# Performance work log

Hardware: AMD Instinct MI355X
Metric: run time of the kernel (lower is better)

The kernel has to match this reference:

```python
import jax, jax.numpy as jnp
import numpy as np

NUM_LAYERS = 3

def setup_inputs() -> dict:
    key = jax.random.key(0)
    k1, k2, k3, k4 = jax.random.split(key, 4)
    N, D, E = 100000, 128, 3200000
    x = jax.random.normal(k1, (N, D), dtype=jnp.float32)
    edge_row = jax.random.randint(k2, (E,), 0, N, dtype=jnp.int64 if jax.config.jax_enable_x64 else jnp.int32)
    edge_col = jax.random.randint(k3, (E,), 0, N, dtype=jnp.int64 if jax.config.jax_enable_x64 else jnp.int32)
    # normalized-adjacency-like positive values
    edge_val = jax.random.uniform(k4, (E,), dtype=jnp.float32)
    return {"x": x, "edge_row": edge_row, "edge_col": edge_col, "edge_val": edge_val}

def _spmm(edge_row, edge_col, edge_val, emb, num_nodes):
    # out[r] += val * emb[c]  -- sparse adjacency @ emb
    msgs = edge_val[:, None] * emb[edge_col]          # [E, D] gather + scale
    return jax.ops.segment_sum(msgs, edge_row, num_segments=num_nodes)

def reference(x, edge_row, edge_col, edge_val):
    N = x.shape[0]
    emb = x
    acc = x  # running sum over layer embeddings (layer 0 included)
    for _ in range(NUM_LAYERS):
        emb = _spmm(edge_row, edge_col, edge_val, emb, N)
        acc = acc + emb
    # mean over (num_layers + 1) stacked embeddings, without materializing the stack
    return acc / jnp.float32(NUM_LAYERS + 1)
```

## Files before the change

kernel.cpp:

```cpp
#include <hip/hip_runtime.h>

#define DIMS 128
#define RPB 64
#define CAP 3072
#define NBK_MAX 1600
#define NBINS 1024

typedef _Float16 half_t;
typedef _Float16 half2_t __attribute__((ext_vector_type(2)));

static __device__ __forceinline__ unsigned halfbits(float v) {
    half_t h = (half_t)v;
    unsigned short us;
    __builtin_memcpy(&us, &h, 2);
    return (unsigned)us;
}

__global__ void cvt_kernel(const float* __restrict__ src, half_t* __restrict__ dst, int n2) {
    int i = blockIdx.x * blockDim.x + threadIdx.x;
    if (i >= n2) return;
    float2 v = reinterpret_cast<const float2*>(src)[i];
    half2_t h;
    h.x = (half_t)v.x;
    h.y = (half_t)v.y;
    reinterpret_cast<half2_t*>(&dst[0])[i] = h;
}

__global__ __launch_bounds__(256) void binA_kernel(
    const int* __restrict__ row, const int* __restrict__ col,
    const float* __restrict__ val, int E, int nbk,
    int* __restrict__ fill, int2* __restrict__ staged) {
    __shared__ int cnt[NBK_MAX];
    __shared__ int base[NBK_MAX];
    const int t = threadIdx.x;
    const int tile0 = blockIdx.x * 8192;
    for (int j = t; j < nbk; j += 256) cnt[j] = 0;
    __syncthreads();
    for (int k = 0; k < 8; ++k) {
        int e = tile0 + (k * 256 + t) * 4;
        if (e + 3 < E) {
            int4 r4 = *reinterpret_cast<const int4*>(&row[e]);
            atomicAdd(&cnt[r4.x >> 6], 1);
            atomicAdd(&cnt[r4.y >> 6], 1);
            atomicAdd(&cnt[r4.z >> 6], 1);
            atomicAdd(&cnt[r4.w >> 6], 1);
        } else {
            for (int j = e; j < E; ++j) atomicAdd(&cnt[row[j] >> 6], 1);
        }
    }
    __syncthreads();
    for (int j = t; j < nbk; j += 256) {
        int c = cnt[j];
        base[j] = c ? atomicAdd(&fill[j], c) : 0;
        cnt[j] = 0;
    }
    __syncthreads();
    for (int k = 0; k < 8; ++k) {
        int e = tile0 + (k * 256 + t) * 4;
        int n = (e + 3 < E) ? 4 : max(0, E - e);
        if (n == 4) {
            int4 r4 = *reinterpret_cast<const int4*>(&row[e]);
            int4 c4 = *reinterpret_cast<const int4*>(&col[e]);
            float4 v4 = *reinterpret_cast<const float4*>(&val[e]);
            int rr[4] = {r4.x, r4.y, r4.z, r4.w};
            int cc[4] = {c4.x, c4.y, c4.z, c4.w};
            float vv[4] = {v4.x, v4.y, v4.z, v4.w};
#pragma unroll
            for (int j = 0; j < 4; ++j) {
                int b = rr[j] >> 6;
                int p = base[b] + atomicAdd(&cnt[b], 1);
                if (p < CAP) {
                    unsigned hb = halfbits(vv[j]);
                    int2 pk;
                    pk.x = (int)(((unsigned)(rr[j] & 63) << 26) | ((unsigned)cc[j] << 8));
                    pk.y = (int)((hb << 16) | hb);
                    staged[(size_t)b * CAP + p] = pk;
                }
            }
        } else {
            for (int j = e; j < e + n; ++j) {
                int r = row[j];
                int b = r >> 6;
                int p = base[b] + atomicAdd(&cnt[b], 1);
                if (p < CAP) {
                    unsigned hb = halfbits(val[j]);
                    int2 pk;
                    pk.x = (int)(((unsigned)(r & 63) << 26) | ((unsigned)col[j] << 8));
                    pk.y = (int)((hb << 16) | hb);
                    staged[(size_t)b * CAP + p] = pk;
                }
            }
        }
    }
}

__global__ __launch_bounds__(512) void sort_bucket(
    const int* __restrict__ fill, int2* __restrict__ staged,
    int* __restrict__ rowinfo, int N) {
    __shared__ int2 buf[CAP];
    __shared__ int2 outb[CAP];
    __shared__ int cur[NBINS];
    __shared__ int wsum[8];
    const int b = blockIdx.x;
    const int t = threadIdx.x;
    const int w = t >> 6, lane = t & 63;
    const int cnt = min(fill[b], CAP);
    int2* gb = staged + (size_t)b * CAP;

    cur[2 * t] = 0;
    cur[2 * t + 1] = 0;
    for (int i = t; i < cnt; i += 512) buf[i] = gb[i];
    __syncthreads();
    for (int i = t; i < cnt; i += 512) {
        unsigned k = (unsigned)buf[i].x;
        int key = (int)((k >> 26) << 4) | (int)((k >> 21) & 0xF);
        atomicAdd(&cur[key], 1);
    }
    __syncthreads();
    int h0 = cur[2 * t], h1 = cur[2 * t + 1];
    int s = h0 + h1;
    int v = s;
    for (int d = 1; d < 64; d <<= 1) {
        int u = __shfl_up(v, d, 64);
        if (lane >= d) v += u;
    }
    if (lane == 63) wsum[w] = v;
    __syncthreads();
    if (t < 8) {
        int ws = wsum[t];
        int vv = ws;
        for (int d = 1; d < 8; d <<= 1) {
            int u = __shfl_up(vv, d, 64);
            if (t >= d) vv += u;
        }
        wsum[t] = vv - ws;
    }
    __syncthreads();
    int excl = wsum[w] + (v - s);
    cur[2 * t] = excl;
    cur[2 * t + 1] = excl + h0;
    __syncthreads();
    if (t < RPB) {
        int start = cur[t * 16];
        int end = (t == RPB - 1) ? cnt : cur[t * 16 + 16];
        int r = b * RPB + t;
        if (r < N) rowinfo[r] = (start << 16) | end;
    }
    __syncthreads();
    for (int i = t; i < cnt; i += 512) {
        int2 pk = buf[i];
        unsigned k = (unsigned)pk.x;
        int key = (int)((k >> 26) << 4) | (int)((k >> 21) & 0xF);
        int p = atomicAdd(&cur[key], 1);
        outb[p] = pk;
    }
    __syncthreads();
    for (int i = t; i < cnt; i += 512) gb[i] = outb[i];
}

template <int MODE>
__global__ __launch_bounds__(256) void spmm_kernel(
    const half_t* __restrict__ emb_in, const int* __restrict__ rowinfo,
    const int2* __restrict__ staged, int N,
    half_t* __restrict__ emb_out, half_t* __restrict__ acc_h,
    float* __restrict__ out) {
    int r = (blockIdx.x * blockDim.x + threadIdx.x) >> 6;
    int lane = threadIdx.x & 63;
    if (r >= N) return;
    int info = rowinfo[r];
    int start = info >> 16;
    int end = info & 0xFFFF;
    const int2* eb = staged + (size_t)(r >> 6) * CAP;
    const char* tbl = reinterpret_cast<const char*>(emb_in);
    const unsigned lane4 = (unsigned)lane << 2;

    half2_t acc[8];
#pragma unroll
    for (int k = 0; k < 8; ++k) acc[k] = (half2_t)0;

    for (int base = start; base < end; base += 64) {
        const int cnt = min(64, end - base);
        int2 myE = make_int2(0, 0);
        if (base + lane < end) myE = eb[base + lane];

        int k = 0;
        for (; k + 7 < cnt; k += 8) {
            int ex[8], ey[8];
#pragma unroll
            for (int j = 0; j < 8; ++j) {
                ex[j] = __shfl(myE.x, k + j, 64);
                ey[j] = __shfl(myE.y, k + j, 64);
            }
            half2_t tv[8];
#pragma unroll
            for (int j = 0; j < 8; ++j) {
                unsigned voff = (((unsigned)ex[j]) & 0x03FFFF00u) + lane4;
                tv[j] = *reinterpret_cast<const half2_t*>(tbl + voff);
            }
#pragma unroll
            for (int j = 0; j < 8; ++j) {
                half2_t vv = __builtin_bit_cast(half2_t, ey[j]);
                acc[j] = tv[j] * vv + acc[j];
            }
        }
        for (; k < cnt; ++k) {
            int ex = __shfl(myE.x, k, 64);
            int ey = __shfl(myE.y, k, 64);
            unsigned voff = (((unsigned)ex) & 0x03FFFF00u) + lane4;
            half2_t tvs = *reinterpret_cast<const half2_t*>(tbl + voff);
            half2_t vv = __builtin_bit_cast(half2_t, ey);
            acc[0] = tvs * vv + acc[0];
        }
    }
    half2_t a01 = acc[0] + acc[1], a23 = acc[2] + acc[3];
    half2_t a45 = acc[4] + acc[5], a67 = acc[6] + acc[7];
    half2_t a = (a01 + a23) + (a45 + a67);

    size_t o = (size_t)r * DIMS + 2 * lane;
    if (MODE == 0 || MODE == 1) {
        *reinterpret_cast<half2_t*>(&emb_out[o]) = a;
    }
    if (MODE == 0) {
        half2_t xv = *reinterpret_cast<const half2_t*>(&emb_in[o]);
        *reinterpret_cast<half2_t*>(&acc_h[o]) = xv + a;
    } else if (MODE == 1) {
        half2_t cv = *reinterpret_cast<half2_t*>(&acc_h[o]);
        *reinterpret_cast<half2_t*>(&acc_h[o]) = cv + a;
    } else {
        half2_t cv = *reinterpret_cast<half2_t*>(&acc_h[o]);
        *reinterpret_cast<float2*>(&out[o]) =
            make_float2(((float)cv.x + (float)a.x) * 0.25f,
                        ((float)cv.y + (float)a.y) * 0.25f);
    }
}


extern "C" void kernel_launch(void* const* d_in, const int* in_sizes, int n_in,
                              void* d_out, int out_size, void* d_ws, size_t ws_size,
                              hipStream_t stream) {
    const float* x = (const float*)d_in[0];
    const int* erow = (const int*)d_in[1];
    const int* ecol = (const int*)d_in[2];
    const float* eval = (const float*)d_in[3];
    const int N = in_sizes[0] / DIMS;
    const int E = in_sizes[1];
    float* out = (float*)d_out;
    const int nbk = (N + RPB - 1) / RPB;

    char* ws = (char*)d_ws;
    size_t off = 0;
    auto carve = [&](size_t bytes) {
        void* p = ws + off;
        off = (off + bytes + 255) & ~(size_t)255;
        return p;
    };
    half_t* xh = (half_t*)carve((size_t)N * DIMS * sizeof(half_t));
    half_t* embB1 = (half_t*)carve((size_t)N * DIMS * sizeof(half_t));
    half_t* acc_h = (half_t*)carve((size_t)N * DIMS * sizeof(half_t));
    int2* staged = (int2*)carve((size_t)nbk * CAP * sizeof(int2));
    int* fill = (int*)carve((size_t)nbk * sizeof(int));
    int* rowinfo = (int*)carve((size_t)N * sizeof(int));
    (void)ws_size;

    hipMemsetAsync(fill, 0, (size_t)nbk * sizeof(int), stream);
    const int n2 = N * DIMS / 2;
    cvt_kernel<<<(n2 + 255) / 256, 256, 0, stream>>>(x, xh, n2);
    binA_kernel<<<(E + 8191) / 8192, 256, 0, stream>>>(erow, ecol, eval, E, nbk, fill, staged);
    sort_bucket<<<nbk, 512, 0, stream>>>(fill, staged, rowinfo, N);

    const int spmm_blocks = (N + 3) / 4;
    spmm_kernel<0><<<spmm_blocks, 256, 0, stream>>>(xh, rowinfo, staged, N, embB1, acc_h, out);
    spmm_kernel<1><<<spmm_blocks, 256, 0, stream>>>(embB1, rowinfo, staged, N, xh, acc_h, out);
    spmm_kernel<2><<<spmm_blocks, 256, 0, stream>>>(xh, rowinfo, staged, N, embB1, acc_h, out);
}
```

Baseline: 541.7 us.

## Fuse first SpMM layer into bucket sort kernel and unroll gather loop to 16

The bucket sort kernel now goes on to compute the first SpMM layer directly from its sorted edges in shared memory. Each wave handles 8 rows and writes emb and acc, which removes one kernel launch and the re-read of the staged edge list from global memory. The remaining SpMM kernels gain a 16-edge unrolled inner loop to put more gathers in flight. The trade-off is that the sort kernel, at 512 threads with large shared memory, now also runs gather work at limited occupancy, and the larger unroll raises register pressure.

```diff
diff --git a/kernel.cpp b/kernel.cpp
--- a/kernel.cpp
+++ b/kernel.cpp
@@ -94,13 +94,16 @@
     }
 }
 
-__global__ __launch_bounds__(512) void sort_bucket(
+__global__ __launch_bounds__(512) void sort_spmm0(
     const int* __restrict__ fill, int2* __restrict__ staged,
-    int* __restrict__ rowinfo, int N) {
+    int* __restrict__ rowinfo, int N,
+    const half_t* __restrict__ xh, half_t* __restrict__ emb_out,
+    half_t* __restrict__ acc_h) {
     __shared__ int2 buf[CAP];
     __shared__ int2 outb[CAP];
     __shared__ int cur[NBINS];
     __shared__ int wsum[8];
+    __shared__ int rinfo[RPB];
     const int b = blockIdx.x;
     const int t = threadIdx.x;
     const int w = t >> 6, lane = t & 63;
@@ -143,6 +146,7 @@
     if (t < RPB) {
         int start = cur[t * 16];
         int end = (t == RPB - 1) ? cnt : cur[t * 16 + 16];
+        rinfo[t] = (start << 16) | end;
         int r = b * RPB + t;
         if (r < N) rowinfo[r] = (start << 16) | end;
     }
@@ -156,6 +160,55 @@
     }
     __syncthreads();
     for (int i = t; i < cnt; i += 512) gb[i] = outb[i];
+
+    const char* tbl = reinterpret_cast<const char*>(xh);
+    const unsigned lane4 = (unsigned)lane << 2;
+#pragma unroll
+    for (int k = 0; k < 8; ++k) {
+        const int rl = w * 8 + k;
+        const int info = rinfo[rl];
+        const int st = info >> 16;
+        const int en = info & 0xFFFF;
+
+        half2_t acc[8];
+#pragma unroll
+        for (int j = 0; j < 8; ++j) acc[j] = (half2_t)0;
+        int e = st;
+        for (; e + 7 < en; e += 8) {
+            int2 p[8];
+#pragma unroll
+            for (int j = 0; j < 8; ++j) p[j] = outb[e + j];
+            half2_t tv[8];
+#pragma unroll
+            for (int j = 0; j < 8; ++j) {
+                unsigned voff = (((unsigned)p[j].x) & 0x03FFFF00u) + lane4;
+                tv[j] = *reinterpret_cast<const half2_t*>(tbl + voff);
+            }
+#pragma unroll
+            for (int j = 0; j < 8; ++j) {
+                half2_t vv = __builtin_bit_cast(half2_t, p[j].y);
+                acc[j] = tv[j] * vv + acc[j];
+            }
+        }
+        for (; e < en; ++e) {
+            int2 p0 = outb[e];
+            unsigned voff = (((unsigned)p0.x) & 0x03FFFF00u) + lane4;
+            half2_t tvs = *reinterpret_cast<const half2_t*>(tbl + voff);
+            half2_t vv = __builtin_bit_cast(half2_t, p0.y);
+            acc[0] = tvs * vv + acc[0];
+        }
+        half2_t a01 = acc[0] + acc[1], a23 = acc[2] + acc[3];
+        half2_t a45 = acc[4] + acc[5], a67 = acc[6] + acc[7];
+        half2_t a = (a01 + a23) + (a45 + a67);
+
+        const int r = b * RPB + rl;
+        if (r < N) {
+            size_t o = (size_t)r * DIMS + 2 * lane;
+            *reinterpret_cast<half2_t*>(&emb_out[o]) = a;
+            half2_t xv = *reinterpret_cast<const half2_t*>(&xh[o]);
+            *reinterpret_cast<half2_t*>(&acc_h[o]) = xv + a;
+        }
+    }
 }
 
 template <int MODE>
@@ -184,6 +237,25 @@
         if (base + lane < end) myE = eb[base + lane];
 
         int k = 0;
+        for (; k + 15 < cnt; k += 16) {
+            int ex[16], ey[16];
+#pragma unroll
+            for (int j = 0; j < 16; ++j) {
+                ex[j] = __shfl(myE.x, k + j, 64);
+                ey[j] = __shfl(myE.y, k + j, 64);
+            }
+            half2_t tv[16];
+#pragma unroll
+            for (int j = 0; j < 16; ++j) {
+                unsigned voff = (((unsigned)ex[j]) & 0x03FFFF00u) + lane4;
+                tv[j] = *reinterpret_cast<const half2_t*>(tbl + voff);
+            }
+#pragma unroll
+            for (int j = 0; j < 16; ++j) {
+                half2_t vv = __builtin_bit_cast(half2_t, ey[j]);
+                acc[j & 7] = tv[j] * vv + acc[j & 7];
+            }
+        }
         for (; k + 7 < cnt; k += 8) {
             int ex[8], ey[8];
 #pragma unroll
@@ -217,13 +289,8 @@
     half2_t a = (a01 + a23) + (a45 + a67);
 
     size_t o = (size_t)r * DIMS + 2 * lane;
-    if (MODE == 0 || MODE == 1) {
+    if (MODE == 1) {
         *reinterpret_cast<half2_t*>(&emb_out[o]) = a;
-    }
-    if (MODE == 0) {
-        half2_t xv = *reinterpret_cast<const half2_t*>(&emb_in[o]);
-        *reinterpret_cast<half2_t*>(&acc_h[o]) = xv + a;
-    } else if (MODE == 1) {
         half2_t cv = *reinterpret_cast<half2_t*>(&acc_h[o]);
         *reinterpret_cast<half2_t*>(&acc_h[o]) = cv + a;
     } else {
@@ -266,10 +333,10 @@
     const int n2 = N * DIMS / 2;
     cvt_kernel<<<(n2 + 255) / 256, 256, 0, stream>>>(x, xh, n2);
     binA_kernel<<<(E + 8191) / 8192, 256, 0, stream>>>(erow, ecol, eval, E, nbk, fill, staged);
-    sort_bucket<<<nbk, 512, 0, stream>>>(fill, staged, rowinfo, N);
+
+    sort_spmm0<<<nbk, 512, 0, stream>>>(fill, staged, rowinfo, N, xh, embB1, acc_h);
 
     const int spmm_blocks = (N + 3) / 4;
-    spmm_kernel<0><<<spmm_blocks, 256, 0, stream>>>(xh, rowinfo, staged, N, embB1, acc_h, out);
     spmm_kernel<1><<<spmm_blocks, 256, 0, stream>>>(embB1, rowinfo, staged, N, xh, acc_h, out);
     spmm_kernel<2><<<spmm_blocks, 256, 0, stream>>>(xh, rowinfo, staged, N, embB1, acc_h, out);
 }
```

New measurement: 553.0 us. 2.1% more time.
